# Optimization experiments

Hardware: AMD Instinct MI355X
Metric: run time of the kernel (lower is better)

Reference implementation:

```python
import jax, jax.numpy as jnp
import numpy as np

NUM_HEADS = 16
ROPE_BASE = 50.0


def _apply_rope(x):
    # x: [b, s, h, d]; torchtune-style rotary embedding with base=ROPE_BASE
    b, s, h, d = x.shape
    inv_freq = 1.0 / (ROPE_BASE ** (jnp.arange(0, d, 2, dtype=jnp.float32) / d))  # [d/2]
    angles = jnp.arange(s, dtype=jnp.float32)[:, None] * inv_freq[None, :]         # [s, d/2]
    cos = jnp.cos(angles)[None, :, None, :]  # [1, s, 1, d/2]
    sin = jnp.sin(angles)[None, :, None, :]
    xr = x.reshape(b, s, h, d // 2, 2)
    x0, x1 = xr[..., 0], xr[..., 1]
    out = jnp.stack([x0 * cos - x1 * sin, x1 * cos + x0 * sin], axis=-1)
    return out.reshape(b, s, h, d).astype(x.dtype)


def setup_inputs() -> dict:
    key = jax.random.key(0)
    k1, k2, k3 = jax.random.split(key, 3)
    B, S, D = 2, 2048, 1024
    x = jax.random.normal(k1, (B, S, D), dtype=jnp.float32)
    w_qkv = jax.random.normal(k2, (3 * D, D), dtype=jnp.float32) * (D ** -0.5)
    w_out = jax.random.normal(k3, (D, D), dtype=jnp.float32) * (D ** -0.5)
    b_out = jnp.zeros((D,), dtype=jnp.float32)
    return {"x": x, "w_qkv": w_qkv, "w_out": w_out, "b_out": b_out}


def reference(x, w_qkv, w_out, b_out):
    B, S, D = x.shape
    H = NUM_HEADS
    dk = D // H

    qkv = x @ w_qkv.T                       # [b, s, 3D]
    q, k, v = jnp.split(qkv, 3, axis=-1)
    q = q.reshape(B, S, H, dk)
    k = k.reshape(B, S, H, dk)
    q = _apply_rope(q)
    k = _apply_rope(k)
    q = q.transpose(0, 2, 1, 3)             # [b, h, s, d]
    k = k.transpose(0, 2, 1, 3)
    v = v.reshape(B, S, H, dk).transpose(0, 2, 1, 3)

    scale = 1.0 / jnp.sqrt(jnp.asarray(dk, dtype=x.dtype))
    scores = jnp.einsum('bhsd,bhtd->bhst', q, k) * scale  # [b, h, s, s]
    # additive diagonal mask: -inf on the diagonal (blocks self-attention)
    eye = jnp.eye(S, dtype=bool)
    scores = jnp.where(eye[None, None], -jnp.inf, scores)
    attn = jax.nn.softmax(scores, axis=-1)
    out = jnp.einsum('bhst,bhtd->bhsd', attn, v)          # [b, h, s, d]
    out = out.transpose(0, 2, 1, 3).reshape(B, S, D)
    return out @ w_out.T + b_out
```

## Files before the change

kernel.cpp:

```cpp
#include <hip/hip_runtime.h>
#include <hip/hip_bf16.h>
#include <math.h>
#include <type_traits>

#define D_MODEL 1024
#define NHEADS  16
#define DK      64
#define SEQ     2048
#define BATCH   2
#define QTILE   128

typedef __attribute__((ext_vector_type(8)))  short  short8;
typedef __attribute__((ext_vector_type(8)))  unsigned short ushort8;
typedef __attribute__((ext_vector_type(4)))  float  floatx4;
typedef __attribute__((ext_vector_type(16))) float  floatx16;

template <int N> using IC = std::integral_constant<int, N>;

__device__ __forceinline__ unsigned short f2bf(float f) {
    union { float f; unsigned int u; } v; v.f = f;
    unsigned int u = v.u;
    return (unsigned short)((u + 0x7FFFu + ((u >> 16) & 1u)) >> 16);
}
__device__ __forceinline__ float bf2f(unsigned short u) {
    union { unsigned int u; float f; } v; v.u = ((unsigned int)u) << 16;
    return v.f;
}
__device__ __forceinline__ unsigned int fau(float f) {
    union { float f; unsigned int u; } v; v.f = f; return v.u;
}

__device__ __forceinline__ void gload_lds16(const unsigned short* g, unsigned short* l) {
    __builtin_amdgcn_global_load_lds((__attribute__((address_space(1))) const void*)g,
                                     (__attribute__((address_space(3))) void*)l,
                                     16, 0, 0);
}

#define X8 ((BATCH * SEQ * D_MODEL) / 8)
#define W8 ((3 * D_MODEL * D_MODEL) / 8)
#define O8 ((D_MODEL * D_MODEL) / 8)
__global__ __launch_bounds__(256) void pack_all(const float* __restrict__ x,
                                                const float* __restrict__ wq,
                                                const float* __restrict__ wo,
                                                unsigned short* __restrict__ xb,
                                                unsigned short* __restrict__ wqb,
                                                unsigned short* __restrict__ wob) {
    const int t = blockIdx.x * blockDim.x + threadIdx.x;
    const float* src; unsigned short* dst; int idx;
    if (t < X8)           { src = x;  dst = xb;  idx = t; }
    else if (t < X8 + W8) { src = wq; dst = wqb; idx = t - X8; }
    else if (t < X8 + W8 + O8) { src = wo; dst = wob; idx = t - X8 - W8; }
    else return;
    const float4 a = ((const float4*)src)[2 * idx];
    const float4 b = ((const float4*)src)[2 * idx + 1];
    short8 o;
    o[0] = (short)f2bf(a.x); o[1] = (short)f2bf(a.y);
    o[2] = (short)f2bf(a.z); o[3] = (short)f2bf(a.w);
    o[4] = (short)f2bf(b.x); o[5] = (short)f2bf(b.y);
    o[6] = (short)f2bf(b.z); o[7] = (short)f2bf(b.w);
    ((short8*)dst)[idx] = o;
}

#define QKV_M 4096
#define QKV_N 3072
#define QKV_K 1024
#define QKV_NT (QKV_K / 64)

__global__ __launch_bounds__(512, 2) void gemm_qkv_8ph(const unsigned short* __restrict__ A,
                                                        const unsigned short* __restrict__ B,
                                                        unsigned short* __restrict__ C) {
    __shared__ __align__(16) unsigned short As[2][256][64];
    __shared__ __align__(16) unsigned short Bs[2][256][64];

    const int tid  = threadIdx.x;
    const int w    = tid >> 6;
    const int lane = tid & 63;
    const int quad = lane >> 4;
    const int lcol = lane & 15;
    const int wr   = w >> 2;
    const int wc   = w & 3;

    const int f  = blockIdx.x;
    const int wg = (f & 7) * 24 + (f >> 3);
    const int tn = (wg % (QKV_N / 256)) * 256;
    const int tm = (wg / (QKV_N / 256)) * 256;

    const int srow8 = lane >> 3;
    const int sj    = lane & 7;

    auto stageA = [&](int buf, int kt, int mh) {
#pragma unroll
        for (int c = 0; c < 2; ++c) {
            const int r0 = mh * 64 + c * 128 + w * 8;
            const int r  = r0 + srow8;
            gload_lds16(A + (size_t)(tm + r) * QKV_K + kt * 64 + ((sj ^ (r & 7)) * 8),
                        &As[buf][r0][0]);
        }
    };
    auto stageB = [&](int buf, int kt, int nh) {
#pragma unroll
        for (int c = 0; c < 2; ++c) {
            const int rho0 = c * 64 + w * 8;
            const int r0   = (rho0 >> 5) * 64 + nh * 32 + (rho0 & 31);
            const int r    = r0 + srow8;
            gload_lds16(B + (size_t)(tn + r) * QKV_K + kt * 64 + ((sj ^ (r & 7)) * 8),
                        &Bs[buf][r0][0]);
        }
    };

    floatx4 acc[8][4];
#pragma unroll
    for (int i = 0; i < 8; ++i)
#pragma unroll
        for (int j = 0; j < 4; ++j) acc[i][j] = (floatx4){0.f, 0.f, 0.f, 0.f};

    auto do_phase = [&](int buf, auto vmc, auto kkc, auto mhc, auto stager) {
        constexpr int VM = decltype(vmc)::value;
        constexpr int kk = decltype(kkc)::value;
        constexpr int mh = decltype(mhc)::value;
        if constexpr (VM == 2) asm volatile("s_waitcnt vmcnt(2)" ::: "memory");
        else                   asm volatile("s_waitcnt vmcnt(4)" ::: "memory");
        __builtin_amdgcn_s_barrier();
        asm volatile("" ::: "memory");
        short8 a[4], b[4];
#pragma unroll
        for (int i = 0; i < 4; ++i) {
            const int r = wr * 128 + mh * 64 + i * 16 + lcol;
            a[i] = *(const short8*)&As[buf][r][((kk * 4 + quad) ^ (r & 7)) * 8];
        }
#pragma unroll
        for (int j = 0; j < 4; ++j) {
            const int r = wc * 64 + j * 16 + lcol;
            b[j] = *(const short8*)&Bs[buf][r][((kk * 4 + quad) ^ (r & 7)) * 8];
        }
        stager();
        __builtin_amdgcn_s_setprio(1);
#pragma unroll
        for (int i = 0; i < 4; ++i)
#pragma unroll
            for (int j = 0; j < 4; ++j)
                acc[mh * 4 + i][j] = __builtin_amdgcn_mfma_f32_16x16x32_bf16(
                    a[i], b[j], acc[mh * 4 + i][j], 0, 0, 0);
        __builtin_amdgcn_s_setprio(0);
    };

    stageB(0, 0, 0); stageB(0, 0, 1); stageA(0, 0, 0); stageA(0, 0, 1);

    for (int t = 0; t < QKV_NT; ++t) {
        const int buf = t & 1, nb = buf ^ 1;
        const int kn = (t + 1 == QKV_NT) ? 0 : t + 1;
        do_phase(buf, IC<2>{}, IC<0>{}, IC<0>{}, [&] { stageB(nb, kn, 0); });
        do_phase(buf, IC<2>{}, IC<0>{}, IC<1>{}, [&] { stageB(nb, kn, 1); });
        do_phase(buf, IC<4>{}, IC<1>{}, IC<0>{}, [&] { stageA(nb, kn, 0); });
        do_phase(buf, IC<4>{}, IC<1>{}, IC<1>{}, [&] { stageA(nb, kn, 1); });
    }

#pragma unroll
    for (int i = 0; i < 8; ++i) {
#pragma unroll
        for (int rr = 0; rr < 4; ++rr) {
            const int row = tm + wr * 128 + i * 16 + quad * 4 + rr;
#pragma unroll
            for (int jf = 0; jf < 4; ++jf) {
                const int col = tn + wc * 64 + jf * 16 + lcol;
                C[(size_t)row * QKV_N + col] = f2bf(acc[i][jf][rr]);
            }
        }
    }
}

#define OUT_M 4096
#define OUT_N 1024
#define OUT_K 1024
#define OUT_NT (OUT_K / 64)

__global__ __launch_bounds__(512, 2) void gemm_out_8ph(const unsigned short* __restrict__ A,
                                                       const unsigned short* __restrict__ B,
                                                       const float* __restrict__ bias,
                                                       float* __restrict__ C) {
    __shared__ __align__(16) unsigned short As[2][128][64];
    __shared__ __align__(16) unsigned short Bs[2][128][64];

    const int tid  = threadIdx.x;
    const int w    = tid >> 6;
    const int lane = tid & 63;
    const int quad = lane >> 4;
    const int lcol = lane & 15;
    const int wr   = w >> 2;
    const int wc   = w & 3;

    const int f  = blockIdx.x;
    const int wg = (f & 7) * 32 + (f >> 3);
    const int tn = (wg & 7) * 128;
    const int tm = (wg >> 3) * 128;

    const int srow8 = lane >> 3;
    const int sj    = lane & 7;

    auto stageA = [&](int buf, int kt, int mh) {
        const int r0 = (w & 3) * 8 + mh * 32 + (w >> 2) * 64;
        const int r  = r0 + srow8;
        gload_lds16(A + (size_t)(tm + r) * OUT_K + kt * 64 + ((sj ^ (r & 7)) * 8),
                    &As[buf][r0][0]);
    };
    auto stageB = [&](int buf, int kt, int nh) {
        const int r0 = (w >> 1) * 32 + nh * 16 + (w & 1) * 8;
        const int r  = r0 + srow8;
        gload_lds16(B + (size_t)(tn + r) * OUT_K + kt * 64 + ((sj ^ (r & 7)) * 8),
                    &Bs[buf][r0][0]);
    };

    floatx4 acc[4][2];
#pragma unroll
    for (int i = 0; i < 4; ++i)
#pragma unroll
        for (int j = 0; j < 2; ++j) acc[i][j] = (floatx4){0.f, 0.f, 0.f, 0.f};

    auto do_phase = [&](int buf, auto vmc, auto kkc, auto mhc, auto stager) {
        constexpr int VM = decltype(vmc)::value;
        constexpr int kk = decltype(kkc)::value;
        constexpr int mh = decltype(mhc)::value;
        if constexpr (VM == 1) asm volatile("s_waitcnt vmcnt(1)" ::: "memory");
        else                   asm volatile("s_waitcnt vmcnt(2)" ::: "memory");
        __builtin_amdgcn_s_barrier();
        asm volatile("" ::: "memory");
        short8 a[2], b[2];
#pragma unroll
        for (int i = 0; i < 2; ++i) {
            const int r = wr * 64 + mh * 32 + i * 16 + lcol;
            a[i] = *(const short8*)&As[buf][r][((kk * 4 + quad) ^ (r & 7)) * 8];
        }
#pragma unroll
        for (int j = 0; j < 2; ++j) {
            const int r = wc * 32 + j * 16 + lcol;
            b[j] = *(const short8*)&Bs[buf][r][((kk * 4 + quad) ^ (r & 7)) * 8];
        }
        stager();
        __builtin_amdgcn_s_setprio(1);
#pragma unroll
        for (int i = 0; i < 2; ++i)
#pragma unroll
            for (int j = 0; j < 2; ++j)
                acc[mh * 2 + i][j] = __builtin_amdgcn_mfma_f32_16x16x32_bf16(
                    a[i], b[j], acc[mh * 2 + i][j], 0, 0, 0);
        __builtin_amdgcn_s_setprio(0);
    };

    stageB(0, 0, 0); stageB(0, 0, 1); stageA(0, 0, 0); stageA(0, 0, 1);

    for (int t = 0; t < OUT_NT; ++t) {
        const int buf = t & 1, nb = buf ^ 1;
        const int kn = (t + 1 == OUT_NT) ? 0 : t + 1;
        do_phase(buf, IC<1>{}, IC<0>{}, IC<0>{}, [&] { stageB(nb, kn, 0); });
        do_phase(buf, IC<1>{}, IC<0>{}, IC<1>{}, [&] { stageB(nb, kn, 1); });
        do_phase(buf, IC<2>{}, IC<1>{}, IC<0>{}, [&] { stageA(nb, kn, 0); });
        do_phase(buf, IC<2>{}, IC<1>{}, IC<1>{}, [&] { stageA(nb, kn, 1); });
    }

#pragma unroll
    for (int i = 0; i < 4; ++i) {
#pragma unroll
        for (int rr = 0; rr < 4; ++rr) {
            const int row = tm + wr * 64 + i * 16 + quad * 4 + rr;
#pragma unroll
            for (int j = 0; j < 2; ++j) {
                const int col = tn + wc * 32 + j * 16 + lcol;
                C[(size_t)row * OUT_N + col] = acc[i][j][rr] + bias[col];
            }
        }
    }
}

__global__ __launch_bounds__(256) void rope_vtrans(const unsigned short* __restrict__ qkvb,
                                                   unsigned short* __restrict__ Qb,
                                                   unsigned short* __restrict__ Kb,
                                                   unsigned short* __restrict__ Vtg) {
    const int st = blockIdx.x, h = blockIdx.y, b = blockIdx.z;
    const int tid = threadIdx.x;
    const int s0 = st * 64;

    const int i  = tid & 31;
    const int r0 = tid >> 5;
    const float inv_freq = exp2f(-(2.0f * (float)i / (float)DK) * log2f(50.0f));
    const float QSCALE = 0.125f * 1.44269504f;
#pragma unroll
    for (int pass = 0; pass < 8; ++pass) {
        const int s = s0 + r0 + pass * 8;
        const size_t in_base = ((size_t)(b * SEQ + s)) * (3 * D_MODEL) + h * DK + 2 * i;
        const float q0 = bf2f(qkvb[in_base]),           q1 = bf2f(qkvb[in_base + 1]);
        const float k0 = bf2f(qkvb[in_base + D_MODEL]), k1 = bf2f(qkvb[in_base + D_MODEL + 1]);
        float sn, cs;
        __sincosf((float)s * inv_freq, &sn, &cs);
        const size_t ob = (((size_t)(b * NHEADS + h)) * SEQ + s) * DK + 2 * i;
        const unsigned int qw = (unsigned int)f2bf((q0 * cs - q1 * sn) * QSCALE)
                              | ((unsigned int)f2bf((q1 * cs + q0 * sn) * QSCALE) << 16);
        const unsigned int kw = (unsigned int)f2bf(k0 * cs - k1 * sn)
                              | ((unsigned int)f2bf(k1 * cs + k0 * sn) << 16);
        *(unsigned int*)&Qb[ob] = qw;
        *(unsigned int*)&Kb[ob] = kw;
    }

    __shared__ unsigned short Lt[64][65];
    const int r = tid >> 3;
    const int c = (tid & 7) * 8;
    const size_t in_row = ((size_t)(b * SEQ + s0 + r)) * (3 * D_MODEL) + 2 * D_MODEL + h * DK + c;
    const ushort8 v0 = *(const ushort8*)&qkvb[in_row];
    const ushort8 v1 = *(const ushort8*)&qkvb[in_row + (size_t)32 * (3 * D_MODEL)];
    const int u0 = r, u1 = r + 32;
    const int kc0 = (u0 & 48) | (8 * ((u0 >> 2) & 1) + (u0 & 3) + 4 * ((u0 >> 3) & 1));
    const int kc1 = (u1 & 48) | (8 * ((u1 >> 2) & 1) + (u1 & 3) + 4 * ((u1 >> 3) & 1));
#pragma unroll
    for (int j = 0; j < 8; ++j) Lt[c + j][kc0] = v0[j];
#pragma unroll
    for (int j = 0; j < 8; ++j) Lt[c + j][kc1] = v1[j];
    __syncthreads();
    const size_t bh = (size_t)(b * NHEADS + h);
    ushort8 o0, o1;
#pragma unroll
    for (int j = 0; j < 8; ++j) { o0[j] = Lt[r][c + j]; o1[j] = Lt[r + 32][c + j]; }
    unsigned short* orow = Vtg + (bh * DK + r) * SEQ + s0 + c;
    *(ushort8*)orow = o0;
    *(ushort8*)(orow + (size_t)32 * SEQ) = o1;
}

#define LDW 72

__global__ __launch_bounds__(512, 4) void flash_attn(const unsigned short* __restrict__ Qb,
                                                     const unsigned short* __restrict__ Kb,
                                                     const unsigned short* __restrict__ Vtg,
                                                     unsigned short* __restrict__ attnb) {
    const int tid  = threadIdx.x;
    const int wave = tid >> 6;
    const int lane = tid & 63;
    const int l31  = lane & 31;
    const int lh   = lane >> 5;
    const int mh2  = wave & 3;
    const int kh   = wave >> 2;
    const int kb   = kh * 32;

    const int f  = blockIdx.x + gridDim.x * (blockIdx.y + gridDim.y * blockIdx.z);
    const int w  = (f & 7) * 64 + (f >> 3);
    const int qt = w & 15;
    const int h  = (w >> 4) & 15;
    const int b  = w >> 8;

    __shared__ __align__(16) unsigned char smem[55296];
    auto KsAt = [&](int s) { return (unsigned short (*)[LDW])(smem + s * 18432); };
    auto VtAt = [&](int s) { return (unsigned short (*)[LDW])(smem + s * 18432 + 9216); };
    float (*Ored)[68] = (float (*)[68])smem;
    float* lred0 = (float*)(smem + 34816);
    float* lred1 = lred0 + 128;

    const size_t bh = (size_t)(b * NHEADS + h);
    const unsigned short* Qg = Qb + (bh * SEQ + (size_t)qt * QTILE) * DK;
    const unsigned short* Kg = Kb + bh * SEQ * DK;
    const unsigned short* Vg = Vtg + bh * (size_t)DK * SEQ;

    short8 qf[4];
#pragma unroll
    for (int t = 0; t < 4; ++t)
        qf[t] = *(const short8*)&Qg[(size_t)(mh2 * 32 + l31) * DK + t * 16 + lh * 8];

    const int strow = tid >> 3;
    const int stcol = (tid & 7) * 8;
    const unsigned short* kg = &Kg[(size_t)strow * DK + stcol];
    const unsigned short* vg = &Vg[(size_t)strow * SEQ + stcol];

    short8 kr = *(const short8*)&kg[0];
    short8 vr = *(const short8*)&vg[0];

    floatx16 oacc[2];
    oacc[0] = (floatx16)(0.f);
    oacc[1] = (floatx16)(0.f);
    float lp = 0.f;

    const int diagkt = qt * QTILE + mh2 * 32 - kb;

    auto finishP = [&](floatx16 s, int kt, unsigned short (*Vt)[LDW]) {
        if (kt == diagkt) {
#pragma unroll
            for (int r = 0; r < 16; ++r) {
                const int key_loc = (r & 3) + 8 * (r >> 2) + 4 * lh;
                if (key_loc == l31) s[r] = -1e30f;
            }
        }
        short8 pf0, pf1;
        {
            union { unsigned int u[4]; short8 s8; } a, c;
#pragma unroll
            for (int d = 0; d < 4; ++d) {
                const float e0 = __builtin_amdgcn_exp2f(s[2 * d]);
                const float e1 = __builtin_amdgcn_exp2f(s[2 * d + 1]);
                a.u[d] = __builtin_amdgcn_perm(fau(e1), fau(e0), 0x07060302u);
                const float f0 = __builtin_amdgcn_exp2f(s[8 + 2 * d]);
                const float f1 = __builtin_amdgcn_exp2f(s[8 + 2 * d + 1]);
                c.u[d] = __builtin_amdgcn_perm(fau(f1), fau(f0), 0x07060302u);
                lp += (e0 + e1) + (f0 + f1);
            }
            pf0 = a.s8;
            pf1 = c.s8;
        }
        __builtin_amdgcn_s_setprio(1);
#pragma unroll
        for (int nd = 0; nd < 2; ++nd) {
            const short8 vfa = *(short8*)&Vt[nd * 32 + l31][kb + lh * 8];
            const short8 vfb = *(short8*)&Vt[nd * 32 + l31][kb + 16 + lh * 8];
            oacc[nd] = __builtin_amdgcn_mfma_f32_32x32x16_bf16(pf0, vfa, oacc[nd], 0, 0, 0);
            oacc[nd] = __builtin_amdgcn_mfma_f32_32x32x16_bf16(pf1, vfb, oacc[nd], 0, 0, 0);
        }
        __builtin_amdgcn_s_setprio(0);
    };

    floatx16 scp;
    int bs = 0, bsp = 0;
    for (int j = 0; j < 32; ++j) {
        unsigned short (*Ks)[LDW] = KsAt(bs);
        *(short8*)&Ks[strow][stcol]        = kr;
        *(short8*)&VtAt(bs)[strow][stcol]  = vr;
        __syncthreads();
        const int ktn = (j + 1 < 32) ? (j + 1) * 64 : 0;
        kr = *(const short8*)&kg[(size_t)ktn * DK];
        vr = *(const short8*)&vg[ktn];

        floatx16 sc = (floatx16)(0.f);
        __builtin_amdgcn_s_setprio(1);
#pragma unroll
        for (int t = 0; t < 4; ++t) {
            const short8 kf = *(short8*)&Ks[kb + l31][t * 16 + lh * 8];
            sc = __builtin_amdgcn_mfma_f32_32x32x16_bf16(kf, qf[t], sc, 0, 0, 0);
        }
        __builtin_amdgcn_s_setprio(0);

        if (j > 0) finishP(scp, (j - 1) * 64, VtAt(bsp));
        scp = sc;
        bsp = bs;
        bs  = (bs == 2) ? 0 : bs + 1;
    }
    finishP(scp, 31 * 64, VtAt(bsp));

    const float lptot = lp + __shfl_xor(lp, 32, 64);

    __syncthreads();
    if (lh == 0) {
        if (kh == 0) lred0[mh2 * 32 + l31] = lptot;
        else         lred1[mh2 * 32 + l31] = lptot;
    }
    if (kh == 1) {
#pragma unroll
        for (int r = 0; r < 16; ++r) {
            const int m = mh2 * 32 + (r & 3) + 8 * (r >> 2) + 4 * lh;
            Ored[m][l31]      = oacc[0][r];
            Ored[m][32 + l31] = oacc[1][r];
        }
    }
    __syncthreads();
    if (kh == 0) {
        unsigned short* obase = attnb + ((size_t)b * SEQ + (size_t)qt * QTILE) * D_MODEL + h * DK;
#pragma unroll
        for (int r = 0; r < 16; ++r) {
            const int m = mh2 * 32 + (r & 3) + 8 * (r >> 2) + 4 * lh;
            const float inv = 1.001953125f / (lred0[m] + lred1[m]);
            const float v0 = (oacc[0][r] + Ored[m][l31]) * inv;
            const float v1 = (oacc[1][r] + Ored[m][32 + l31]) * inv;
            obase[(size_t)m * D_MODEL + l31]      = f2bf(v0);
            obase[(size_t)m * D_MODEL + 32 + l31] = f2bf(v1);
        }
    }
}

extern "C" void kernel_launch(void* const* d_in, const int* in_sizes, int n_in,
                              void* d_out, int out_size, void* d_ws, size_t ws_size,
                              hipStream_t stream) {
    const float* x     = (const float*)d_in[0];
    const float* w_qkv = (const float*)d_in[1];
    const float* w_out = (const float*)d_in[2];
    const float* b_out = (const float*)d_in[3];
    float* out = (float*)d_out;

    const int M = BATCH * SEQ;
    const size_t X_ELEMS    = (size_t)M * D_MODEL;
    const size_t WQKV_ELEMS = (size_t)3 * D_MODEL * D_MODEL;
    const size_t WOUT_ELEMS = (size_t)D_MODEL * D_MODEL;
    const size_t QKV_ELEMS  = (size_t)M * 3 * D_MODEL;
    const size_t HEAD_ELEMS = (size_t)BATCH * NHEADS * SEQ * DK;

    unsigned short* xb    = (unsigned short*)d_ws;
    unsigned short* wqkvb = xb + X_ELEMS;
    unsigned short* woutb = wqkvb + WQKV_ELEMS;
    unsigned short* qkvb  = woutb + WOUT_ELEMS;
    unsigned short* Qb    = qkvb + QKV_ELEMS;
    unsigned short* Kb    = Qb + HEAD_ELEMS;
    unsigned short* Vtg   = Kb + HEAD_ELEMS;
    unsigned short* attnb = Vtg + HEAD_ELEMS;

    pack_all<<<(X8 + W8 + O8 + 255) / 256, 256, 0, stream>>>(x, w_qkv, w_out, xb, wqkvb, woutb);

    gemm_qkv_8ph<<<(QKV_M / 256) * (QKV_N / 256), 512, 0, stream>>>(xb, wqkvb, qkvb);

    {
        dim3 grid(SEQ / 64, NHEADS, BATCH);
        rope_vtrans<<<grid, 256, 0, stream>>>(qkvb, Qb, Kb, Vtg);
    }
    {
        dim3 grid(SEQ / QTILE, NHEADS, BATCH);
        flash_attn<<<grid, 512, 0, stream>>>(Qb, Kb, Vtg, attnb);
    }
    gemm_out_8ph<<<(OUT_M / 128) * (OUT_N / 128), 512, 0, stream>>>(attnb, woutb, b_out, out);
}
```

Baseline: 184.5 us.

## Double query tile to 256 and give each wave full key tiles

New measurement: 182.8 us. Within noise of the previous version (-0.9%).

```diff
diff --git a/kernel.cpp b/kernel.cpp
--- a/kernel.cpp
+++ b/kernel.cpp
@@ -8,7 +8,7 @@
 #define DK      64
 #define SEQ     2048
 #define BATCH   2
-#define QTILE   128
+#define QTILE   256
 
 typedef __attribute__((ext_vector_type(8)))  short  short8;
 typedef __attribute__((ext_vector_type(8)))  unsigned short ushort8;
@@ -325,31 +325,27 @@
 
 #define LDW 72
 
-__global__ __launch_bounds__(512, 4) void flash_attn(const unsigned short* __restrict__ Qb,
+__global__ __launch_bounds__(512, 2) void flash_attn(const unsigned short* __restrict__ Qb,
                                                      const unsigned short* __restrict__ Kb,
                                                      const unsigned short* __restrict__ Vtg,
                                                      unsigned short* __restrict__ attnb) {
     const int tid  = threadIdx.x;
-    const int wave = tid >> 6;
+    const int w8   = tid >> 6;
     const int lane = tid & 63;
     const int l31  = lane & 31;
     const int lh   = lane >> 5;
-    const int mh2  = wave & 3;
-    const int kh   = wave >> 2;
-    const int kb   = kh * 32;
 
     const int f  = blockIdx.x + gridDim.x * (blockIdx.y + gridDim.y * blockIdx.z);
-    const int w  = (f & 7) * 64 + (f >> 3);
-    const int qt = w & 15;
-    const int h  = (w >> 4) & 15;
-    const int b  = w >> 8;
-
-    __shared__ __align__(16) unsigned char smem[55296];
-    auto KsAt = [&](int s) { return (unsigned short (*)[LDW])(smem + s * 18432); };
-    auto VtAt = [&](int s) { return (unsigned short (*)[LDW])(smem + s * 18432 + 9216); };
-    float (*Ored)[68] = (float (*)[68])smem;
-    float* lred0 = (float*)(smem + 34816);
-    float* lred1 = lred0 + 128;
+    const int w  = (f & 7) * 32 + (f >> 3);
+    const int qt = w & 7;
+    const int h  = (w >> 3) & 15;
+    const int b  = w >> 7;
+
+    __shared__ __align__(16) unsigned char smem[36864];
+    unsigned short (*Ks0)[LDW] = (unsigned short (*)[LDW])(smem);
+    unsigned short (*Vt0)[LDW] = (unsigned short (*)[LDW])(smem +  9216);
+    unsigned short (*Ks1)[LDW] = (unsigned short (*)[LDW])(smem + 18432);
+    unsigned short (*Vt1)[LDW] = (unsigned short (*)[LDW])(smem + 27648);
 
     const size_t bh = (size_t)(b * NHEADS + h);
     const unsigned short* Qg = Qb + (bh * SEQ + (size_t)qt * QTILE) * DK;
@@ -359,7 +355,7 @@
     short8 qf[4];
 #pragma unroll
     for (int t = 0; t < 4; ++t)
-        qf[t] = *(const short8*)&Qg[(size_t)(mh2 * 32 + l31) * DK + t * 16 + lh * 8];
+        qf[t] = *(const short8*)&Qg[(size_t)(w8 * 32 + l31) * DK + t * 16 + lh * 8];
 
     const int strow = tid >> 3;
     const int stcol = (tid & 7) * 8;
@@ -374,97 +370,88 @@
     oacc[1] = (floatx16)(0.f);
     float lp = 0.f;
 
-    const int diagkt = qt * QTILE + mh2 * 32 - kb;
-
-    auto finishP = [&](floatx16 s, int kt, unsigned short (*Vt)[LDW]) {
+    const int diagkt = qt * QTILE + (w8 >> 1) * 64;
+    const int dH     = w8 & 1;
+
+    auto compute = [&](unsigned short (*Ks)[LDW], unsigned short (*Vt)[LDW], int kt) {
+        floatx16 sc0 = (floatx16)(0.f), sc1 = (floatx16)(0.f);
+        __builtin_amdgcn_s_setprio(1);
+#pragma unroll
+        for (int t = 0; t < 4; ++t) {
+            const short8 kf0 = *(short8*)&Ks[l31][t * 16 + lh * 8];
+            const short8 kf1 = *(short8*)&Ks[32 + l31][t * 16 + lh * 8];
+            sc0 = __builtin_amdgcn_mfma_f32_32x32x16_bf16(kf0, qf[t], sc0, 0, 0, 0);
+            sc1 = __builtin_amdgcn_mfma_f32_32x32x16_bf16(kf1, qf[t], sc1, 0, 0, 0);
+        }
+        __builtin_amdgcn_s_setprio(0);
+
         if (kt == diagkt) {
 #pragma unroll
             for (int r = 0; r < 16; ++r) {
                 const int key_loc = (r & 3) + 8 * (r >> 2) + 4 * lh;
-                if (key_loc == l31) s[r] = -1e30f;
+                if (key_loc == l31) { if (dH) sc1[r] = -1e30f; else sc0[r] = -1e30f; }
             }
         }
-        short8 pf0, pf1;
+
+        short8 pf[4];
         {
-            union { unsigned int u[4]; short8 s8; } a, c;
+            union { unsigned int u[4]; short8 s8; } g0, g1, g2, g3;
 #pragma unroll
             for (int d = 0; d < 4; ++d) {
-                const float e0 = __builtin_amdgcn_exp2f(s[2 * d]);
-                const float e1 = __builtin_amdgcn_exp2f(s[2 * d + 1]);
-                a.u[d] = __builtin_amdgcn_perm(fau(e1), fau(e0), 0x07060302u);
-                const float f0 = __builtin_amdgcn_exp2f(s[8 + 2 * d]);
-                const float f1 = __builtin_amdgcn_exp2f(s[8 + 2 * d + 1]);
-                c.u[d] = __builtin_amdgcn_perm(fau(f1), fau(f0), 0x07060302u);
-                lp += (e0 + e1) + (f0 + f1);
+                const float a0 = __builtin_amdgcn_exp2f(sc0[2 * d]);
+                const float a1 = __builtin_amdgcn_exp2f(sc0[2 * d + 1]);
+                g0.u[d] = __builtin_amdgcn_perm(fau(a1), fau(a0), 0x07060302u);
+                const float b0 = __builtin_amdgcn_exp2f(sc0[8 + 2 * d]);
+                const float b1 = __builtin_amdgcn_exp2f(sc0[8 + 2 * d + 1]);
+                g1.u[d] = __builtin_amdgcn_perm(fau(b1), fau(b0), 0x07060302u);
+                const float c0 = __builtin_amdgcn_exp2f(sc1[2 * d]);
+                const float c1 = __builtin_amdgcn_exp2f(sc1[2 * d + 1]);
+                g2.u[d] = __builtin_amdgcn_perm(fau(c1), fau(c0), 0x07060302u);
+                const float d0 = __builtin_amdgcn_exp2f(sc1[8 + 2 * d]);
+                const float d1 = __builtin_amdgcn_exp2f(sc1[8 + 2 * d + 1]);
+                g3.u[d] = __builtin_amdgcn_perm(fau(d1), fau(d0), 0x07060302u);
+                lp += ((a0 + a1) + (b0 + b1)) + ((c0 + c1) + (d0 + d1));
             }
-            pf0 = a.s8;
-            pf1 = c.s8;
-        }
+            pf[0] = g0.s8; pf[1] = g1.s8; pf[2] = g2.s8; pf[3] = g3.s8;
+        }
+
         __builtin_amdgcn_s_setprio(1);
 #pragma unroll
-        for (int nd = 0; nd < 2; ++nd) {
-            const short8 vfa = *(short8*)&Vt[nd * 32 + l31][kb + lh * 8];
-            const short8 vfb = *(short8*)&Vt[nd * 32 + l31][kb + 16 + lh * 8];
-            oacc[nd] = __builtin_amdgcn_mfma_f32_32x32x16_bf16(pf0, vfa, oacc[nd], 0, 0, 0);
-            oacc[nd] = __builtin_amdgcn_mfma_f32_32x32x16_bf16(pf1, vfb, oacc[nd], 0, 0, 0);
-        }
+        for (int nd = 0; nd < 2; ++nd)
+#pragma unroll
+            for (int ks = 0; ks < 4; ++ks) {
+                const short8 vf = *(short8*)&Vt[nd * 32 + l31][ks * 16 + lh * 8];
+                oacc[nd] = __builtin_amdgcn_mfma_f32_32x32x16_bf16(pf[ks], vf, oacc[nd], 0, 0, 0);
+            }
         __builtin_amdgcn_s_setprio(0);
     };
 
-    floatx16 scp;
-    int bs = 0, bsp = 0;
-    for (int j = 0; j < 32; ++j) {
-        unsigned short (*Ks)[LDW] = KsAt(bs);
-        *(short8*)&Ks[strow][stcol]        = kr;
-        *(short8*)&VtAt(bs)[strow][stcol]  = vr;
+    for (int kt = 0; kt < SEQ; kt += 128) {
+        *(short8*)&Ks0[strow][stcol] = kr;
+        *(short8*)&Vt0[strow][stcol] = vr;
         __syncthreads();
-        const int ktn = (j + 1 < 32) ? (j + 1) * 64 : 0;
+        kr = *(const short8*)&kg[(size_t)(kt + 64) * DK];
+        vr = *(const short8*)&vg[kt + 64];
+        compute(Ks0, Vt0, kt);
+
+        *(short8*)&Ks1[strow][stcol] = kr;
+        *(short8*)&Vt1[strow][stcol] = vr;
+        __syncthreads();
+        const int ktn = (kt + 128 < SEQ) ? kt + 128 : 0;
         kr = *(const short8*)&kg[(size_t)ktn * DK];
         vr = *(const short8*)&vg[ktn];
-
-        floatx16 sc = (floatx16)(0.f);
-        __builtin_amdgcn_s_setprio(1);
-#pragma unroll
-        for (int t = 0; t < 4; ++t) {
-            const short8 kf = *(short8*)&Ks[kb + l31][t * 16 + lh * 8];
-            sc = __builtin_amdgcn_mfma_f32_32x32x16_bf16(kf, qf[t], sc, 0, 0, 0);
-        }
-        __builtin_amdgcn_s_setprio(0);
-
-        if (j > 0) finishP(scp, (j - 1) * 64, VtAt(bsp));
-        scp = sc;
-        bsp = bs;
-        bs  = (bs == 2) ? 0 : bs + 1;
-    }
-    finishP(scp, 31 * 64, VtAt(bsp));
+        compute(Ks1, Vt1, kt + 64);
+    }
 
     const float lptot = lp + __shfl_xor(lp, 32, 64);
-
-    __syncthreads();
-    if (lh == 0) {
-        if (kh == 0) lred0[mh2 * 32 + l31] = lptot;
-        else         lred1[mh2 * 32 + l31] = lptot;
-    }
-    if (kh == 1) {
-#pragma unroll
-        for (int r = 0; r < 16; ++r) {
-            const int m = mh2 * 32 + (r & 3) + 8 * (r >> 2) + 4 * lh;
-            Ored[m][l31]      = oacc[0][r];
-            Ored[m][32 + l31] = oacc[1][r];
-        }
-    }
-    __syncthreads();
-    if (kh == 0) {
-        unsigned short* obase = attnb + ((size_t)b * SEQ + (size_t)qt * QTILE) * D_MODEL + h * DK;
-#pragma unroll
-        for (int r = 0; r < 16; ++r) {
-            const int m = mh2 * 32 + (r & 3) + 8 * (r >> 2) + 4 * lh;
-            const float inv = 1.001953125f / (lred0[m] + lred1[m]);
-            const float v0 = (oacc[0][r] + Ored[m][l31]) * inv;
-            const float v1 = (oacc[1][r] + Ored[m][32 + l31]) * inv;
-            obase[(size_t)m * D_MODEL + l31]      = f2bf(v0);
-            obase[(size_t)m * D_MODEL + 32 + l31] = f2bf(v1);
-        }
+    unsigned short* obase = attnb + ((size_t)b * SEQ + (size_t)qt * QTILE + w8 * 32) * D_MODEL
+                          + h * DK;
+#pragma unroll
+    for (int r = 0; r < 16; ++r) {
+        const int mq = (r & 3) + 8 * (r >> 2) + 4 * lh;
+        const float inv = 1.001953125f / __shfl(lptot, mq, 64);
+        obase[(size_t)mq * D_MODEL + l31]      = f2bf(oacc[0][r] * inv);
+        obase[(size_t)mq * D_MODEL + 32 + l31] = f2bf(oacc[1][r] * inv);
     }
 }
 
```

## Replace triple-buffered software-pipelined attention loop with double-buffered unrolled loop

Applied to the files above, without the earlier changes.

Result: no change. 184.6 us (+0.0%).

```diff
diff --git a/kernel.cpp b/kernel.cpp
--- a/kernel.cpp
+++ b/kernel.cpp
@@ -287,8 +287,12 @@
     for (int pass = 0; pass < 8; ++pass) {
         const int s = s0 + r0 + pass * 8;
         const size_t in_base = ((size_t)(b * SEQ + s)) * (3 * D_MODEL) + h * DK + 2 * i;
-        const float q0 = bf2f(qkvb[in_base]),           q1 = bf2f(qkvb[in_base + 1]);
-        const float k0 = bf2f(qkvb[in_base + D_MODEL]), k1 = bf2f(qkvb[in_base + D_MODEL + 1]);
+        const unsigned int qin = *(const unsigned int*)&qkvb[in_base];
+        const unsigned int kin = *(const unsigned int*)&qkvb[in_base + D_MODEL];
+        const float q0 = bf2f((unsigned short)(qin & 0xFFFFu));
+        const float q1 = bf2f((unsigned short)(qin >> 16));
+        const float k0 = bf2f((unsigned short)(kin & 0xFFFFu));
+        const float k1 = bf2f((unsigned short)(kin >> 16));
         float sn, cs;
         __sincosf((float)s * inv_freq, &sn, &cs);
         const size_t ob = (((size_t)(b * NHEADS + h)) * SEQ + s) * DK + 2 * i;
@@ -344,9 +348,11 @@
     const int h  = (w >> 4) & 15;
     const int b  = w >> 8;
 
-    __shared__ __align__(16) unsigned char smem[55296];
-    auto KsAt = [&](int s) { return (unsigned short (*)[LDW])(smem + s * 18432); };
-    auto VtAt = [&](int s) { return (unsigned short (*)[LDW])(smem + s * 18432 + 9216); };
+    __shared__ __align__(16) unsigned char smem[36864];
+    unsigned short (*Ks0)[LDW] = (unsigned short (*)[LDW])(smem);
+    unsigned short (*Vt0)[LDW] = (unsigned short (*)[LDW])(smem +  9216);
+    unsigned short (*Ks1)[LDW] = (unsigned short (*)[LDW])(smem + 18432);
+    unsigned short (*Vt1)[LDW] = (unsigned short (*)[LDW])(smem + 27648);
     float (*Ored)[68] = (float (*)[68])smem;
     float* lred0 = (float*)(smem + 34816);
     float* lred1 = lred0 + 128;
@@ -376,30 +382,41 @@
 
     const int diagkt = qt * QTILE + mh2 * 32 - kb;
 
-    auto finishP = [&](floatx16 s, int kt, unsigned short (*Vt)[LDW]) {
+    auto compute = [&](unsigned short (*Ks)[LDW], unsigned short (*Vt)[LDW], int kt) {
+        floatx16 sc = (floatx16)(0.f);
+        __builtin_amdgcn_s_setprio(1);
+#pragma unroll
+        for (int t = 0; t < 4; ++t) {
+            const short8 kf = *(short8*)&Ks[kb + l31][t * 16 + lh * 8];
+            sc = __builtin_amdgcn_mfma_f32_32x32x16_bf16(kf, qf[t], sc, 0, 0, 0);
+        }
+        __builtin_amdgcn_s_setprio(0);
+
         if (kt == diagkt) {
 #pragma unroll
             for (int r = 0; r < 16; ++r) {
                 const int key_loc = (r & 3) + 8 * (r >> 2) + 4 * lh;
-                if (key_loc == l31) s[r] = -1e30f;
+                if (key_loc == l31) sc[r] = -1e30f;
             }
         }
+
         short8 pf0, pf1;
         {
             union { unsigned int u[4]; short8 s8; } a, c;
 #pragma unroll
             for (int d = 0; d < 4; ++d) {
-                const float e0 = __builtin_amdgcn_exp2f(s[2 * d]);
-                const float e1 = __builtin_amdgcn_exp2f(s[2 * d + 1]);
+                const float e0 = __builtin_amdgcn_exp2f(sc[2 * d]);
+                const float e1 = __builtin_amdgcn_exp2f(sc[2 * d + 1]);
                 a.u[d] = __builtin_amdgcn_perm(fau(e1), fau(e0), 0x07060302u);
-                const float f0 = __builtin_amdgcn_exp2f(s[8 + 2 * d]);
-                const float f1 = __builtin_amdgcn_exp2f(s[8 + 2 * d + 1]);
+                const float f0 = __builtin_amdgcn_exp2f(sc[8 + 2 * d]);
+                const float f1 = __builtin_amdgcn_exp2f(sc[8 + 2 * d + 1]);
                 c.u[d] = __builtin_amdgcn_perm(fau(f1), fau(f0), 0x07060302u);
                 lp += (e0 + e1) + (f0 + f1);
             }
             pf0 = a.s8;
             pf1 = c.s8;
         }
+
         __builtin_amdgcn_s_setprio(1);
 #pragma unroll
         for (int nd = 0; nd < 2; ++nd) {
@@ -411,32 +428,22 @@
         __builtin_amdgcn_s_setprio(0);
     };
 
-    floatx16 scp;
-    int bs = 0, bsp = 0;
-    for (int j = 0; j < 32; ++j) {
-        unsigned short (*Ks)[LDW] = KsAt(bs);
-        *(short8*)&Ks[strow][stcol]        = kr;
-        *(short8*)&VtAt(bs)[strow][stcol]  = vr;
+    for (int kt = 0; kt < SEQ; kt += 128) {
+        *(short8*)&Ks0[strow][stcol] = kr;
+        *(short8*)&Vt0[strow][stcol] = vr;
         __syncthreads();
-        const int ktn = (j + 1 < 32) ? (j + 1) * 64 : 0;
+        kr = *(const short8*)&kg[(size_t)(kt + 64) * DK];
+        vr = *(const short8*)&vg[kt + 64];
+        compute(Ks0, Vt0, kt);
+
+        *(short8*)&Ks1[strow][stcol] = kr;
+        *(short8*)&Vt1[strow][stcol] = vr;
+        __syncthreads();
+        const int ktn = (kt + 128 < SEQ) ? kt + 128 : 0;
         kr = *(const short8*)&kg[(size_t)ktn * DK];
         vr = *(const short8*)&vg[ktn];
-
-        floatx16 sc = (floatx16)(0.f);
-        __builtin_amdgcn_s_setprio(1);
-#pragma unroll
-        for (int t = 0; t < 4; ++t) {
-            const short8 kf = *(short8*)&Ks[kb + l31][t * 16 + lh * 8];
-            sc = __builtin_amdgcn_mfma_f32_32x32x16_bf16(kf, qf[t], sc, 0, 0, 0);
-        }
-        __builtin_amdgcn_s_setprio(0);
-
-        if (j > 0) finishP(scp, (j - 1) * 64, VtAt(bsp));
-        scp = sc;
-        bsp = bs;
-        bs  = (bs == 2) ? 0 : bs + 1;
-    }
-    finishP(scp, 31 * 64, VtAt(bsp));
+        compute(Ks1, Vt1, kt + 64);
+    }
 
     const float lptot = lp + __shfl_xor(lp, 32, 64);
 
```
